# Optimization experiments

Hardware: AMD Instinct MI355X
Metric: run time of the kernel (lower is better)

The kernel has to match this reference:

```python
import jax, jax.numpy as jnp
import numpy as np

H = W = 128
C = 256
NC = 15
BASE_SIZE = 8.0
SCALE = 4.0
RING = np.array([0, 1, 2, 5, 8, 7, 6, 3])  # clockwise ring of 3x3 kernel (row-major idx)
BIAS_CLS = float(-np.log((1.0 - 0.01) / 0.01))  # bias_init_with_prob(0.01)


def conv(x, w, b, pad):
    y = jax.lax.conv_general_dilated(x, w, (1, 1), [(pad, pad), (pad, pad)],
                                     dimension_numbers=('NCHW', 'OIHW', 'NCHW'))
    return y + b[None, :, None, None]


def conv_relu(x, w, b):
    return jax.nn.relu(conv(x, w, b, 1))


def gen_grid_anchors(h, w, stride):
    # AnchorGeneratorRotated: base anchor centered at 0.5*(base_size-1), shifted by stride grid
    ctr = 0.5 * (BASE_SIZE - 1.0)
    gx = jnp.arange(w, dtype=jnp.float32) * stride
    gy = jnp.arange(h, dtype=jnp.float32) * stride
    yy, xx = jnp.meshgrid(gy, gx, indexing='ij')  # row-major (y outer, x inner)
    size = BASE_SIZE * SCALE
    return jnp.stack([xx + ctr, yy + ctr,
                      jnp.full_like(xx, size), jnp.full_like(xx, size),
                      jnp.zeros_like(xx)], axis=-1).reshape(-1, 5)


def norm_angle(a):
    PI = np.pi
    return ((a + PI / 4.0) % PI) - PI / 4.0  # into [-pi/4, 3pi/4)


def rboxes_decode(anchors, deltas, wh_ratio_clip=1e-6):
    # anchors [HW,5], deltas [N,HW,5] -> [N,HW,5]
    max_ratio = float(np.abs(np.log(wh_ratio_clip)))
    dx, dy, dw, dh, dt = [deltas[..., i] for i in range(5)]
    dw = jnp.clip(dw, -max_ratio, max_ratio)
    dh = jnp.clip(dh, -max_ratio, max_ratio)
    ax, ay, aw, ah, aa = [anchors[..., i] for i in range(5)]
    cos, sin = jnp.cos(aa), jnp.sin(aa)
    gx = dx * aw * cos - dy * ah * sin + ax
    gy = dx * aw * sin + dy * ah * cos + ay
    gw = aw * jnp.exp(dw)
    gh = ah * jnp.exp(dh)
    ga = norm_angle(aa + dt)
    return jnp.stack([gx, gy, gw, gh, ga], axis=-1)


def bilinear_sample(x, ys, xs):
    # x [N,C,H,W]; ys/xs [N,H,W,K] float pixel coords -> [N,C,H,W,K], zero outside
    N, Cc, h, w = x.shape
    K = ys.shape[-1]
    x0 = jnp.floor(xs)
    y0 = jnp.floor(ys)
    wx1 = xs - x0
    wx0 = 1.0 - wx1
    wy1 = ys - y0
    wy0 = 1.0 - wy1
    xf = x.reshape(N, Cc, h * w)

    def gather(yi, wy, xi, wxx):
        valid = (yi >= 0) & (yi < h) & (xi >= 0) & (xi < w)
        yc = jnp.clip(yi, 0, h - 1).astype(jnp.int32)
        xc = jnp.clip(xi, 0, w - 1).astype(jnp.int32)
        idx = (yc * w + xc).reshape(N, -1)  # [N,H*W*K]
        v = jax.vmap(lambda xi_, ii_: jnp.take(xi_, ii_, axis=1))(xf, idx)
        v = v.reshape(N, Cc, h, w, K)
        wgt = jnp.where(valid, wy * wxx, 0.0)[:, None]  # [N,1,H,W,K]
        return v * wgt

    out = gather(y0, wy0, x0, wx0)
    out = out + gather(y0, wy0, x0 + 1.0, wx1)
    out = out + gather(y0 + 1.0, wy1, x0, wx0)
    out = out + gather(y0 + 1.0, wy1, x0 + 1.0, wx1)
    return out


def align_conv(x, refine_anchor, stride, w, b):
    # deformable 3x3 conv; sampling grid from refined rotated anchors
    N, Cc, h, ww = x.shape
    k = 3
    idx = jnp.arange(-1, 2, dtype=x.dtype)
    yy, xx = jnp.meshgrid(idx, idx, indexing='ij')
    xx = xx.reshape(-1)
    yy = yy.reshape(-1)  # [9] kernel offsets, row-major matching OIHW flatten
    axc, ayc, aw, ah, aa = [refine_anchor[..., i] for i in range(5)]
    s = jnp.asarray(stride, x.dtype)
    axc, ayc, aw, ah = axc / s, ayc / s, aw / s, ah / s
    cos, sin = jnp.cos(aa), jnp.sin(aa)
    dx = (aw / k)[..., None] * xx  # [N,h,w,9]
    dy = (ah / k)[..., None] * yy
    xs = cos[..., None] * dx - sin[..., None] * dy + axc[..., None]
    ys = sin[..., None] * dx + cos[..., None] * dy + ayc[..., None]
    sampled = bilinear_sample(x, ys, xs)  # [N,C,h,w,9]
    out = jnp.einsum('nchwk,ock->nohw', sampled, w.reshape(w.shape[0], Cc, 9))
    return jax.nn.relu(out + b[None, :, None, None])


def or_conv(x, w, b):
    # ORConv2d(256->32, arf_config=(1,8)): 8 spatially-rotated copies of each 3x3 filter
    o, ci = w.shape[0], w.shape[1]
    wf = w.reshape(o, ci, 9)
    rotated = []
    for r in range(8):
        src = np.arange(9)
        for j in range(8):
            src[RING[j]] = RING[(j - r) % 8]  # rotate ring by r*45deg, center fixed
        rotated.append(wf[..., src])
    wr = jnp.stack(rotated, axis=1).reshape(o * 8, ci, 3, 3)  # channel = o*8 + r
    br = jnp.repeat(b, 8)
    return conv(x, wr, br, 1)


def setup_inputs() -> dict:
    key = jax.random.key(0)
    ks = iter(jax.random.split(key, 32))
    d = {}
    d['feats'] = jax.random.normal(next(ks), (1, C, H, W), dtype=jnp.float32)
    def wlike(shape):
        return 0.01 * jax.random.normal(next(ks), shape, dtype=jnp.float32)
    d['fam_reg_w0'] = wlike((C, C, 3, 3)); d['fam_reg_b0'] = jnp.zeros((C,), jnp.float32)
    d['fam_reg_w1'] = wlike((C, C, 3, 3)); d['fam_reg_b1'] = jnp.zeros((C,), jnp.float32)
    d['fam_reg_hw'] = wlike((5, C, 1, 1)); d['fam_reg_hb'] = jnp.zeros((5,), jnp.float32)
    d['fam_cls_w0'] = wlike((C, C, 3, 3)); d['fam_cls_b0'] = jnp.zeros((C,), jnp.float32)
    d['fam_cls_w1'] = wlike((C, C, 3, 3)); d['fam_cls_b1'] = jnp.zeros((C,), jnp.float32)
    d['fam_cls_hw'] = wlike((NC, C, 1, 1)); d['fam_cls_hb'] = jnp.full((NC,), BIAS_CLS, jnp.float32)
    d['align_w'] = wlike((C, C, 3, 3)); d['align_b'] = jnp.zeros((C,), jnp.float32)
    d['or_w'] = wlike((C // 8, C, 3, 3)); d['or_b'] = jnp.zeros((C // 8,), jnp.float32)
    d['odm_reg_w0'] = wlike((C, C, 3, 3)); d['odm_reg_b0'] = jnp.zeros((C,), jnp.float32)
    d['odm_reg_w1'] = wlike((C, C, 3, 3)); d['odm_reg_b1'] = jnp.zeros((C,), jnp.float32)
    d['odm_reg_hw'] = wlike((5, C, 3, 3)); d['odm_reg_hb'] = jnp.zeros((5,), jnp.float32)
    d['odm_cls_w0'] = wlike((C, C // 8, 3, 3)); d['odm_cls_b0'] = jnp.zeros((C,), jnp.float32)
    d['odm_cls_w1'] = wlike((C, C, 3, 3)); d['odm_cls_b1'] = jnp.zeros((C,), jnp.float32)
    d['odm_cls_hw'] = wlike((NC, C, 3, 3)); d['odm_cls_hb'] = jnp.full((NC,), BIAS_CLS, jnp.float32)
    d['stride'] = 8
    return d


def reference(feats, fam_reg_w0, fam_reg_b0, fam_reg_w1, fam_reg_b1, fam_reg_hw, fam_reg_hb,
              fam_cls_w0, fam_cls_b0, fam_cls_w1, fam_cls_b1, fam_cls_hw, fam_cls_hb,
              align_w, align_b, or_w, or_b,
              odm_reg_w0, odm_reg_b0, odm_reg_w1, odm_reg_b1, odm_reg_hw, odm_reg_hb,
              odm_cls_w0, odm_cls_b0, odm_cls_w1, odm_cls_b1, odm_cls_hw, odm_cls_hb,
              stride):
    x = feats
    t = conv_relu(conv_relu(x, fam_reg_w0, fam_reg_b0), fam_reg_w1, fam_reg_b1)
    fam_bbox_pred = conv(t, fam_reg_hw, fam_reg_hb, 0)  # [N,5,h,w]
    t = conv_relu(conv_relu(x, fam_cls_w0, fam_cls_b0), fam_cls_w1, fam_cls_b1)
    fam_cls_pred = conv(t, fam_cls_hw, fam_cls_hb, 0)   # [N,NC,h,w]
    N, _, h, w = fam_bbox_pred.shape
    anchors = gen_grid_anchors(h, w, stride)  # [h*w,5]
    deltas = jax.lax.stop_gradient(fam_bbox_pred).transpose(0, 2, 3, 1).reshape(N, -1, 5)
    refine_anchor = rboxes_decode(anchors, deltas).reshape(N, h, w, 5)
    al = align_conv(x, refine_anchor, stride, align_w, align_b)  # [N,256,h,w]
    orf = or_conv(al, or_w, or_b)                                # [N,256,h,w]
    pooled = orf.reshape(N, -1, 8, h, w).max(axis=2)             # rotation-invariant pooling -> [N,32,h,w]
    t = conv_relu(conv_relu(pooled, odm_cls_w0, odm_cls_b0), odm_cls_w1, odm_cls_b1)
    odm_cls_pred = conv(t, odm_cls_hw, odm_cls_hb, 1)
    t = conv_relu(conv_relu(orf, odm_reg_w0, odm_reg_b0), odm_reg_w1, odm_reg_b1)
    odm_bbox_pred = conv(t, odm_reg_hw, odm_reg_hb, 1)
    return (fam_cls_pred, fam_bbox_pred, odm_cls_pred, odm_bbox_pred, anchors, refine_anchor)
```

## Files before the change

### kernel.cpp

```cpp
#include <hip/hip_runtime.h>
#include <hip/hip_bf16.h>
#include <hip/hip_fp16.h>

#define HW 128
#define NPX 16384
#define CC 256

typedef short  bf16x8  __attribute__((ext_vector_type(8)));
typedef short  short4v __attribute__((ext_vector_type(4)));
typedef float  f32x4   __attribute__((ext_vector_type(4)));
typedef unsigned int u32x4 __attribute__((ext_vector_type(4)));

static __device__ __forceinline__ short f2bs(float v) {
    union { float f; unsigned u; } x; x.f = v;
    unsigned r = x.u + 0x7FFFu + ((x.u >> 16) & 1u);
    return (short)(r >> 16);
}
static __device__ __forceinline__ float bs2f(short s) {
    union { unsigned u; float f; } x; x.u = ((unsigned)(unsigned short)s) << 16;
    return x.f;
}

static __device__ __forceinline__ int bx_swz() {
    return ((blockIdx.x & 7) << 5) | (blockIdx.x >> 3);
}

struct F8 { unsigned char b; };
__device__ __forceinline__ unsigned char enc8(float v) {
    unsigned short u = __half_as_ushort(__float2half(v));
    unsigned short s = u & 0x8000, mag = u & 0x7FFF;
    mag = (unsigned short)(mag + 0x0080);
    return (unsigned char)((unsigned short)(s | mag) >> 8);
}
__device__ __forceinline__ float dec8(F8 v) {
    return __half2float(__ushort_as_half((unsigned short)(v.b) << 8));
}
__device__ __forceinline__ float ldg_(const float* p) { return *p; }
__device__ __forceinline__ float ldg_(const F8* p)    { return dec8(*p); }

__constant__ int c_ROT9[8][9] = {
    {0,1,2,3,4,5,6,7,8},
    {3,0,1,6,4,2,7,8,5},
    {6,3,0,7,4,1,8,5,2},
    {7,6,3,8,4,0,5,2,1},
    {8,7,6,5,4,3,2,1,0},
    {5,8,7,2,4,6,1,0,3},
    {2,5,8,1,4,7,0,3,6},
    {1,2,5,0,4,8,3,6,7},
};

__device__ __forceinline__ void v9_decode_px(
    const float* bbox, int px, float s,
    float& gx, float& gy, float& gw, float& gh, float& ga)
{
    int y = px >> 7, x = px & 127;
    float ax = x * s + 3.5f, ay = y * s + 3.5f;
    float dx = bbox[0 * NPX + px];
    float dy = bbox[1 * NPX + px];
    float dw = bbox[2 * NPX + px];
    float dh = bbox[3 * NPX + px];
    float dt = bbox[4 * NPX + px];
    const float maxr = 13.815510558f;
    dw = fminf(fmaxf(dw, -maxr), maxr);
    dh = fminf(fmaxf(dh, -maxr), maxr);
    gx = dx * 32.f + ax;
    gy = dy * 32.f + ay;
    gw = 32.f * expf(dw);
    gh = 32.f * expf(dh);
    const float PI = 3.14159265358979323846f;
    float m = fmodf(dt + PI * 0.25f, PI);
    if (m < 0.f) m += PI;
    ga = m - PI * 0.25f;
}


__global__ __launch_bounds__(256) void v10_transpose(
    const float* __restrict__ f, short* __restrict__ xt)
{
    __shared__ float tile[32][33];
    int px0 = blockIdx.x * 32, ci0 = blockIdx.y * 32;
    int tx = threadIdx.x & 31, ty = threadIdx.x >> 5;
#pragma unroll
    for (int i = 0; i < 4; ++i) {
        int ci = ty + i * 8;
        tile[ci][tx] = f[(size_t)(ci0 + ci) * NPX + px0 + tx];
    }
    __syncthreads();
#pragma unroll
    for (int i = 0; i < 4; ++i) {
        int pxr = ty + i * 8;
        xt[(size_t)(px0 + pxr) * 256 + ci0 + tx] = f2bs(tile[tx][pxr]);
    }
}
// ... 126 lines not shown
#pragma unroll
        for (int i = 0; i < 4; ++i)
            if (lofs[i] >= 0) *(bf16x8*)(&S[lofs[i]]) = st[i];
    }
    bf16x8 a[9][OCG];
#pragma unroll
    for (int t = (ONLY1 ? 4 : 0); t < (ONLY1 ? 5 : 9); ++t)
#pragma unroll
        for (int g = 0; g < OCG; ++g)
            a[t][g] = *(const bf16x8*)(wb +
                ((size_t)(t * OCP + ocw + g * 16 + l15) * CIN + quad * 8));
    __syncthreads();

    const int NST = CIN / 32;
    int cur = 0;
    for (int s = 0; s < NST; ++s) {
        const int cib = s * 32;

        bf16x8 st[4];
        if (s + 1 < NST) {
#pragma unroll
            for (int i = 0; i < 4; ++i) {
                st[i] = zf;
                if (gofs[i] >= 0)
                    st[i] = *(const bf16x8*)(xin + gofs[i] + cib + 32);
            }
        }

#pragma unroll
        for (int t = (ONLY1 ? 4 : 0); t < (ONLY1 ? 5 : 9); ++t) {
            const int r = t / 3, dxk = t % 3 - 1;
#pragma unroll
            for (int p = 0; p < 4; ++p) {
                int c = 1 + p * 16 + l15 + dxk;
                bf16x8 b = *(const bf16x8*)(&S[cur * 7920 + (r * 66 + c) * 40 + quad * 8]);
#pragma unroll
                for (int g = 0; g < OCG; ++g)
                    acc[p][g] = __builtin_amdgcn_mfma_f32_16x16x32_bf16(a[t][g], b, acc[p][g], 0, 0, 0);
            }
            if (s + 1 < NST) {
#pragma unroll
                for (int g = 0; g < OCG; ++g)
                    a[t][g] = *(const bf16x8*)(wb +
                        ((size_t)(t * OCP + ocw + g * 16 + l15) * CIN + cib + 32 + quad * 8));
            }
        }

        if (s + 1 < NST) {
#pragma unroll
            for (int i = 0; i < 4; ++i)
                if (lofs[i] >= 0) *(bf16x8*)(&S[(cur ^ 1) * 7920 + lofs[i]]) = st[i];
        }
        __syncthreads();
        cur ^= 1;
    }

#pragma unroll
    for (int p = 0; p < 4; ++p) {
        const int px = y * HW + xh + p * 16 + l15;
#pragma unroll
        for (int g = 0; g < OCG; ++g) {
            const int ocq = ocw + g * 16 + quad * 4;
            if (HEAD) {
                float* o = (float*)outv;
#pragma unroll
                for (int r = 0; r < 4; ++r)
                    if (ocq + r < CoutAct)
                        o[(size_t)(ocq + r) * NPX + px] = acc[p][g][r] + bb[ocq + r];
            } else {
                short4v s4;
#pragma unroll
                for (int r = 0; r < 4; ++r) {
                    float v = acc[p][g][r] + bb[ocq + r];
                    if (RELU) v = fmaxf(v, 0.f);
                    s4[r] = f2bs(v);
                }
                *(short4v*)((short*)outv + (size_t)px * 256 + ocq) = s4;
            }
        }
    }
}

template <int RELU, int CIN>
__device__ __forceinline__ void conv_body4(
    short* S,
    const short* __restrict__ xin, const short* __restrict__ wb,
    const float* __restrict__ bb, short* __restrict__ outb, int bx)
{
    const int y    = bx >> 1;
    const int xh   = (bx & 1) * 64;
    const int tid  = threadIdx.x;
    const int wv   = tid >> 6;
    const int lane = tid & 63;
    const int quad = lane >> 4;
    const int l15  = lane & 15;
    const int ocw  = wv * 64;

    int gofs[4], lofs[4];
#pragma unroll
    for (int i = 0; i < 4; ++i) {
        int e = tid + i * 256;
        gofs[i] = -1; lofs[i] = -1;
        if (e < 792) {
            int pos = e >> 2, part = e & 3;
            int r = pos / 66, c = pos - r * 66;
            int yy = y - 1 + r, xx = xh - 1 + c;
            lofs[i] = (r * 66 + c) * 40 + part * 8;
            if (yy >= 0 && yy < HW && xx >= 0 && xx < HW)
                gofs[i] = (yy * HW + xx) * CIN + part * 8;
        }
    }
    const bf16x8 zf = (bf16x8){0, 0, 0, 0, 0, 0, 0, 0};

    f32x4 acc[4][4];
#pragma unroll
    for (int p = 0; p < 4; ++p)
#pragma unroll
        for (int g = 0; g < 4; ++g) acc[p][g] = (f32x4){0.f, 0.f, 0.f, 0.f};

    {
        bf16x8 st[4];
#pragma unroll
        for (int i = 0; i < 4; ++i) {
            st[i] = zf;
            if (gofs[i] >= 0) st[i] = *(const bf16x8*)(xin + gofs[i]);
        }
#pragma unroll
        for (int i = 0; i < 4; ++i)
            if (lofs[i] >= 0) *(bf16x8*)(&S[lofs[i]]) = st[i];
    }
    bf16x8 aC[4], aN[4];
#pragma unroll
    for (int g = 0; g < 4; ++g)
        aC[g] = *(const bf16x8*)(wb +
            ((size_t)(ocw + g * 16 + l15) * CIN + quad * 8));
#pragma unroll
    for (int g = 0; g < 4; ++g) aN[g] = aC[g];
    __syncthreads();

    const int NST = CIN / 32;
    int cur = 0;
    for (int s = 0; s < NST; ++s) {
        const int cib = s * 32;

        bf16x8 st[4];
        if (s + 1 < NST) {
#pragma unroll
            for (int i = 0; i < 4; ++i) {
                st[i] = zf;
                if (gofs[i] >= 0)
                    st[i] = *(const bf16x8*)(xin + gofs[i] + cib + 32);
            }
        }

#pragma unroll
        for (int t = 0; t < 9; ++t) {
            const int nt   = (t == 8) ? 0 : t + 1;
            const int ncib = (t == 8) ? cib + 32 : cib;
            if (!(s == NST - 1 && t == 8)) {
#pragma unroll
                for (int g = 0; g < 4; ++g)
                    aN[g] = *(const bf16x8*)(wb +
                        ((size_t)(nt * 256 + ocw + g * 16 + l15) * CIN + ncib + quad * 8));
            }
            const int r = t / 3, dxk = t % 3 - 1;
#pragma unroll
            for (int p = 0; p < 4; ++p) {
                int c = 1 + p * 16 + l15 + dxk;
                bf16x8 b = *(const bf16x8*)(&S[cur * 7920 + (r * 66 + c) * 40 + quad * 8]);
#pragma unroll
                for (int g = 0; g < 4; ++g)
                    acc[p][g] = __builtin_amdgcn_mfma_f32_16x16x32_bf16(aC[g], b, acc[p][g], 0, 0, 0);
            }
#pragma unroll
            for (int g = 0; g < 4; ++g) aC[g] = aN[g];
        }

        if (s + 1 < NST) {
#pragma unroll
            for (int i = 0; i < 4; ++i)
                if (lofs[i] >= 0) *(bf16x8*)(&S[(cur ^ 1) * 7920 + lofs[i]]) = st[i];
        }
        __syncthreads();
        cur ^= 1;
    }

#pragma unroll
    for (int p = 0; p < 4; ++p) {
        const int px = y * HW + xh + p * 16 + l15;
#pragma unroll
        for (int g = 0; g < 4; ++g) {
            const int ocq = ocw + g * 16 + quad * 4;
            short4v s4;
#pragma unroll
            for (int r = 0; r < 4; ++r) {
                float v = acc[p][g][r] + bb[ocq + r];
                if (RELU) v = fmaxf(v, 0.f);
                s4[r] = f2bs(v);
            }
            *(short4v*)(outb + (size_t)px * 256 + ocq) = s4;
        }
    }
}

template <int RELU, int HEAD, int ONLY1, int CIN, int OCG>
__global__ __launch_bounds__(256) void v13_conv(
    const short* __restrict__ xin, const short* __restrict__ wb,
    const float* __restrict__ bb, void* __restrict__ outv,
    int CoutAct, int OCP)
{
    __shared__ short S[2 * 7920];
    conv_body<RELU, HEAD, ONLY1, CIN, OCG>(S, xin, wb, bb, outv,
                                           CoutAct, OCP, bx_swz(), blockIdx.y);
}

template <int RELU, int HEAD, int ONLY1, int CIN0, int CIN1, int OCG, int NY, int OCP>
__global__ __launch_bounds__(256) void v13_pair(
    const short* __restrict__ in0, const short* __restrict__ in1,
    const short* __restrict__ wb0, const short* __restrict__ wb1,
    const float* __restrict__ bb0, const float* __restrict__ bb1,
    void* __restrict__ out0, void* __restrict__ out1,
    int cout0, int cout1)
{
    __shared__ short S[2 * 7920];
    const int ybr = blockIdx.y;
    if (ybr < NY)
        conv_body<RELU, HEAD, ONLY1, CIN0, OCG>(S, in0, wb0, bb0, out0,
                                                cout0, OCP, bx_swz(), ybr);
    else
        conv_body<RELU, HEAD, ONLY1, CIN1, OCG>(S, in1, wb1, bb1, out1,
                                                cout1, OCP, bx_swz(), ybr - NY);
}

template <int RELU, int CIN>
__global__ __launch_bounds__(256) __attribute__((amdgpu_waves_per_eu(2, 2)))
void v14_conv(
    const short* __restrict__ xin, const short* __restrict__ wb,
    const float* __restrict__ bb, short* __restrict__ outb)
{
    __shared__ short S[2 * 7920];
    conv_body4<RELU, CIN>(S, xin, wb, bb, outb, bx_swz());
}

template <int RELU, int CIN0, int CIN1>
__global__ __launch_bounds__(256) __attribute__((amdgpu_waves_per_eu(2, 2)))
void v14_pair(
    const short* __restrict__ in0, const short* __restrict__ in1,
    const short* __restrict__ wb0, const short* __restrict__ wb1,
    const float* __restrict__ bb0, const float* __restrict__ bb1,
    short* __restrict__ out0, short* __restrict__ out1)
{
    __shared__ short S[2 * 7920];
    if (blockIdx.y == 0)
        conv_body4<RELU, CIN0>(S, in0, wb0, bb0, out0, bx_swz());
    else
        conv_body4<RELU, CIN1>(S, in1, wb1, bb1, out1, bx_swz());
}

__global__ __launch_bounds__(256) void v13_align(
    const short* __restrict__ xt, const float* __restrict__ bbox,
    const short* __restrict__ wb, const float* __restrict__ bb,
    const int* __restrict__ stride_p, short* __restrict__ outa)
{
    const int bx   = bx_swz();
    const int y    = bx >> 1;
    const int xh   = (bx & 1) * 64;
    const int ocb  = blockIdx.y * 128;
    const int tid  = threadIdx.x;
    const int wv   = tid >> 6, lane = tid & 63, quad = lane >> 4, l15 = lane & 15;
    const int ocw  = ocb + wv * 32;

    __shared__ int   s_idx[4][576];
    __shared__ float s_wgt[4][576];
    __shared__ short S[2][64 * 40];

    const float s = (float)(*stride_p);
    for (int e = tid; e < 576; e += 256) {
        int t = e >> 6, xi = e & 63;
        int px = y * HW + xh + xi;
        float gx, gy, gw, gh, ga;
        v9_decode_px(bbox, px, s, gx, gy, gw, gh, ga);
        float axc = gx / s, ayc = gy / s;
        float aw3 = gw / (3.f * s), ah3 = gh / (3.f * s);
        float cs = cosf(ga), sn = sinf(ga);
        float kx = (float)(t % 3 - 1), ky = (float)(t / 3 - 1);
        float ddx = aw3 * kx, ddy = ah3 * ky;
        float xf = cs * ddx - sn * ddy + axc;
        float yf = sn * ddx + cs * ddy + ayc;
        float fx = floorf(xf), fy = floorf(yf);
        int ix = (int)fx, iy = (int)fy;
        float wx1 = xf - fx, wx0 = 1.f - wx1;
        float wy1 = yf - fy, wy0 = 1.f - wy1;
        bool x0v = (ix >= 0) && (ix < HW), x1v = (ix + 1 >= 0) && (ix + 1 < HW);
        bool y0v = (iy >= 0) && (iy < HW), y1v = (iy + 1 >= 0) && (iy + 1 < HW);
        int x0c = min(max(ix, 0), HW - 1), x1c = min(max(ix + 1, 0), HW - 1);
        int y0c = min(max(iy, 0), HW - 1), y1c = min(max(iy + 1, 0), HW - 1);
        s_idx[0][e] = y0c * HW + x0c;
        s_idx[1][e] = y0c * HW + x1c;
        s_idx[2][e] = y1c * HW + x0c;
        s_idx[3][e] = y1c * HW + x1c;
        s_wgt[0][e] = (y0v && x0v) ? wy0 * wx0 : 0.f;
        s_wgt[1][e] = (y0v && x1v) ? wy0 * wx1 : 0.f;
        s_wgt[2][e] = (y1v && x0v) ? wy1 * wx0 : 0.f;
        s_wgt[3][e] = (y1v && x1v) ? wy1 * wx1 : 0.f;
    }

    f32x4 acc[4][2];
#pragma unroll
    for (int p = 0; p < 4; ++p) { acc[p][0] = (f32x4){0,0,0,0}; acc[p][1] = (f32x4){0,0,0,0}; }

    const int spx = tid >> 2;
    const int sq  = tid & 3;
    const int sw  = spx * 40 + sq * 8;
    const bf16x8 zf = (bf16x8){0, 0, 0, 0, 0, 0, 0, 0};

    __syncthreads();

    bf16x8 aC0, aC1;
    bf16x8 gN0, gN1, gN2, gN3;
    float  wN0, wN1, wN2, wN3;
    {
        int e = spx;
        int i0 = s_idx[0][e], i1 = s_idx[1][e], i2 = s_idx[2][e], i3 = s_idx[3][e];
        float w0 = s_wgt[0][e], w1 = s_wgt[1][e], w2 = s_wgt[2][e], w3 = s_wgt[3][e];
        const short* base = xt + sq * 8;
        bf16x8 g0 = *(const bf16x8*)(base + (size_t)i0 * 256);
        bf16x8 g1 = *(const bf16x8*)(base + (size_t)i1 * 256);
        bf16x8 g2 = *(const bf16x8*)(base + (size_t)i2 * 256);
        bf16x8 g3 = *(const bf16x8*)(base + (size_t)i3 * 256);
        float v[8];
#pragma unroll
        for (int i = 0; i < 8; ++i)
            v[i] = w0 * bs2f(g0[i]) + w1 * bs2f(g1[i]) + w2 * bs2f(g2[i]) + w3 * bs2f(g3[i]);
        u32x4 r;
#pragma unroll
        for (int i = 0; i < 4; ++i)
            asm("v_cvt_pk_bf16_f32 %0, %1, %2" : "=v"(r[i]) : "v"(v[2 * i]), "v"(v[2 * i + 1]));
        *(u32x4*)(&S[0][sw]) = r;
    }
// ... 286 lines not shown
            bool xv1 = (ix + 1 >= 0) && (ix + 1 < HW);
            bool yv0 = (iy >= 0) && (iy < HW);
            bool yv1 = (iy + 1 >= 0) && (iy + 1 < HW);
            if (yv0 && xv0) v += ip[iy * HW + ix] * wy0 * wx0;
            if (yv0 && xv1) v += ip[iy * HW + ix + 1] * wy0 * wx1;
            if (yv1 && xv0) v += ip[(iy + 1) * HW + ix] * wy1 * wx0;
            if (yv1 && xv1) v += ip[(iy + 1) * HW + ix + 1] * wy1 * wx1;
            smp[t >> 7][t & 127] = v;
        }
        __syncthreads();

        float wv[4][9];
#pragma unroll
        for (int i = 0; i < 4; ++i) {
            const float* wp = w + ((size_t)(oc0 + i) * CC + ci) * 9;
#pragma unroll
            for (int k = 0; k < 9; ++k) wv[i][k] = wp[k];
        }
#pragma unroll
        for (int k = 0; k < 9; ++k) {
            float iv[8];
#pragma unroll
            for (int j = 0; j < 8; ++j) iv[j] = smp[k][x0 + j];
#pragma unroll
            for (int i = 0; i < 4; ++i)
#pragma unroll
                for (int j = 0; j < 8; ++j)
                    acc[i][j] += iv[j] * wv[i][k];
        }
    }
#pragma unroll
    for (int i = 0; i < 4; ++i) {
        float b = bias[oc0 + i];
#pragma unroll
        for (int j = 0; j < 8; ++j)
            out[(size_t)(oc0 + i) * NPX + y * HW + x0 + j].b =
                enc8(fmaxf(acc[i][j] + b, 0.f));
    }
}

__global__ __launch_bounds__(256) void v9_pool(
    const F8* __restrict__ orf, F8* __restrict__ pooled)
{
    int g = blockIdx.x * 256 + threadIdx.x;
    if (g >= 32 * NPX) return;
    int px = g & (NPX - 1);
    int c  = g >> 14;
    float m = -3.4e38f;
#pragma unroll
    for (int r = 0; r < 8; ++r)
        m = fmaxf(m, dec8(orf[(size_t)(c * 8 + r) * NPX + px]));
    pooled[g].b = enc8(m);
}

extern "C" void kernel_launch(void* const* d_in, const int* in_sizes, int n_in,
                              void* d_out, int out_size, void* d_ws, size_t ws_size,
                              hipStream_t stream)
{
    const float* feats = (const float*)d_in[0];
    const float* frw0 = (const float*)d_in[1];  const float* frb0 = (const float*)d_in[2];
    const float* frw1 = (const float*)d_in[3];  const float* frb1 = (const float*)d_in[4];
    const float* frhw = (const float*)d_in[5];  const float* frhb = (const float*)d_in[6];
    const float* fcw0 = (const float*)d_in[7];  const float* fcb0 = (const float*)d_in[8];
    const float* fcw1 = (const float*)d_in[9];  const float* fcb1 = (const float*)d_in[10];
    const float* fchw = (const float*)d_in[11]; const float* fchb = (const float*)d_in[12];
    const float* alw  = (const float*)d_in[13]; const float* alb  = (const float*)d_in[14];
    const float* orw  = (const float*)d_in[15]; const float* orb  = (const float*)d_in[16];
    const float* drw0 = (const float*)d_in[17]; const float* drb0 = (const float*)d_in[18];
    const float* drw1 = (const float*)d_in[19]; const float* drb1 = (const float*)d_in[20];
    const float* drhw = (const float*)d_in[21]; const float* drhb = (const float*)d_in[22];
    const float* dcw0 = (const float*)d_in[23]; const float* dcb0 = (const float*)d_in[24];
    const float* dcw1 = (const float*)d_in[25]; const float* dcb1 = (const float*)d_in[26];
    const float* dchw = (const float*)d_in[27]; const float* dchb = (const float*)d_in[28];
    const int*  stride_p = (const int*)d_in[29];

    float* out = (float*)d_out;
    float* o_fam_cls  = out;
    float* o_fam_bbox = out + 245760;
    float* o_odm_cls  = out + 327680;
    float* o_odm_bbox = out + 573440;
    float* o_anchors  = out + 655360;
    float* o_refine   = out + 737280;

    dim3 blk(256);

    const size_t NEED3     = 55097344;
    const size_t NEED2     = 38172672;
    const size_t NEED_FAST = 27395072;
    const size_t NEED_V9   = 8912896;

    if (ws_size >= NEED3) {
        char* ws = (char*)d_ws;
        short* xt = (short*)(ws + 0);
        short* T0 = (short*)(ws + 8388608);
        short* T1 = (short*)(ws + 16777216);
        short* T2 = (short*)(ws + 25165824);
        short* T3 = (short*)(ws + 33554432);
        short* P  = (short*)(ws + 41943040);
        short* WA = (short*)(ws + 42991616);
        float* BA = (float*)(ws + 55083008);

        v12_prepall<<<dim3(2304, 14), blk, 0, stream>>>(
            frw0, frw1, fcw0, fcw1, alw, orw, drw0, drw1, dcw1,
            frhw, fchw, drhw, dchw, dcw0,
            frb0, frb1, fcb0, fcb1, alb, orb, drb0, drb1, dcb1,
            frhb, fchb, drhb, dchb, dcb0,
            WA, BA);
        v10_transpose<<<dim3(512, 8), blk, 0, stream>>>(feats, xt);

        v14_pair<1, 256, 256><<<dim3(256, 2), blk, 0, stream>>>(
            xt, xt, WA + 0, WA + 1179648, BA + 0 * 256, BA + 2 * 256, T0, T2);
        v14_pair<1, 256, 256><<<dim3(256, 2), blk, 0, stream>>>(
            T0, T2, WA + 589824, WA + 1769472, BA + 1 * 256, BA + 3 * 256, T1, T3);
        v13_pair<0, 1, 1, 256, 256, 1, 1, 64><<<dim3(256, 2), blk, 0, stream>>>(
            T1, T3, WA + 5308416, WA + 5455872, BA + 9 * 256, BA + 10 * 256,
            o_fam_bbox, o_fam_cls, 5, 15);
        v9_decode<<<dim3(64), blk, 0, stream>>>(o_fam_bbox, o_anchors, o_refine, stride_p);
        v13_align<<<dim3(256, 2), blk, 0, stream>>>(xt, o_fam_bbox, WA + 2359296, BA + 4 * 256, stride_p, T0);
        v14_conv<0, 256><<<dim3(256, 1), blk, 0, stream>>>(T0, WA + 2949120, BA + 5 * 256, T1);
        v10_pool<<<dim3(2048), blk, 0, stream>>>(T1, P);
        v14_pair<1, 256, 32><<<dim3(256, 2), blk, 0, stream>>>(
            T1, P, WA + 3538944, WA + 5898240, BA + 6 * 256, BA + 13 * 256, T0, T2);
        v14_pair<1, 256, 256><<<dim3(256, 2), blk, 0, stream>>>(
            T0, T2, WA + 4128768, WA + 4718592, BA + 7 * 256, BA + 8 * 256, T1, T3);
        v13_pair<0, 1, 0, 256, 256, 1, 1, 64><<<dim3(256, 2), blk, 0, stream>>>(
            T1, T3, WA + 5603328, WA + 5750784, BA + 11 * 256, BA + 12 * 256,
            o_odm_bbox, o_odm_cls, 5, 15);
    } else if (ws_size >= NEED2) {
        char* ws = (char*)d_ws;
        short* xt = (short*)(ws + 0);
        short* T0 = (short*)(ws + 8388608);
        short* T1 = (short*)(ws + 16777216);
        short* P  = (short*)(ws + 25165824);
        short* WA = (short*)(ws + 26214400);
        float* BA = (float*)(ws + 38158336);

        dim3 gc(256, 2), gh(256, 1);

        v12_prepall<<<dim3(2304, 14), blk, 0, stream>>>(
            frw0, frw1, fcw0, fcw1, alw, orw, drw0, drw1, dcw1,
            frhw, fchw, drhw, dchw, dcw0,
            frb0, frb1, fcb0, fcb1, alb, orb, drb0, drb1, dcb1,
            frhb, fchb, drhb, dchb, dcb0,
            WA, BA);
        v10_transpose<<<dim3(512, 8), blk, 0, stream>>>(feats, xt);

        v13_conv<1, 0, 0, 256, 2><<<gc, blk, 0, stream>>>(xt, WA + 0,       BA + 0 * 256, T0, 256, 256);
        v13_conv<1, 0, 0, 256, 2><<<gc, blk, 0, stream>>>(T0, WA + 589824,  BA + 1 * 256, T1, 256, 256);
        v13_conv<0, 1, 1, 256, 1><<<gh, blk, 0, stream>>>(T1, WA + 5308416, BA + 9 * 256, o_fam_bbox, 5, 64);
        v13_conv<1, 0, 0, 256, 2><<<gc, blk, 0, stream>>>(xt, WA + 1179648, BA + 2 * 256, T0, 256, 256);
        v13_conv<1, 0, 0, 256, 2><<<gc, blk, 0, stream>>>(T0, WA + 1769472, BA + 3 * 256, T1, 256, 256);
        v13_conv<0, 1, 1, 256, 1><<<gh, blk, 0, stream>>>(T1, WA + 5455872, BA + 10 * 256, o_fam_cls, 15, 64);
        v9_decode<<<dim3(64), blk, 0, stream>>>(o_fam_bbox, o_anchors, o_refine, stride_p);
        v13_align<<<dim3(256, 2), blk, 0, stream>>>(xt, o_fam_bbox, WA + 2359296, BA + 4 * 256, stride_p, T0);
        v13_conv<0, 0, 0, 256, 2><<<gc, blk, 0, stream>>>(T0, WA + 2949120, BA + 5 * 256, T1, 256, 256);
        v10_pool<<<dim3(2048), blk, 0, stream>>>(T1, P);
        v13_conv<1, 0, 0, 256, 2><<<gc, blk, 0, stream>>>(T1, WA + 3538944, BA + 6 * 256, T0, 256, 256);
        v13_conv<1, 0, 0, 256, 2><<<gc, blk, 0, stream>>>(T0, WA + 4128768, BA + 7 * 256, T1, 256, 256);
        v13_conv<0, 1, 0, 256, 1><<<gh, blk, 0, stream>>>(T1, WA + 5603328, BA + 11 * 256, o_odm_bbox, 5, 64);
        v13_conv<1, 0, 0, 32, 2><<<gc, blk, 0, stream>>>(P, WA + 5898240, BA + 13 * 256, T0, 256, 256);
        v13_conv<1, 0, 0, 256, 2><<<gc, blk, 0, stream>>>(T0, WA + 4718592, BA + 8 * 256, T1, 256, 256);
        v13_conv<0, 1, 0, 256, 1><<<gh, blk, 0, stream>>>(T1, WA + 5750784, BA + 12 * 256, o_odm_cls, 15, 64);
    } else if (ws_size >= NEED_FAST) {
        char* ws = (char*)d_ws;
        short* xt = (short*)(ws + 0);
        short* T0 = (short*)(ws + 8388608);
        short* T1 = (short*)(ws + 16777216);
        short* P  = (short*)(ws + 25165824);
        short* WB = (short*)(ws + 26214400);
        float* BB = (float*)(ws + 27394048);

        dim3 gc(256, 2), gh(256, 1);

        v10_transpose<<<dim3(512, 8), blk, 0, stream>>>(feats, xt);

#define PREP(W, B, COUT, CIN, OCP, MODE) \
        v10_prep<<<dim3((9 * (OCP) * (CIN) + 255) / 256), blk, 0, stream>>>( \
            W, B, WB, BB, COUT, CIN, OCP, MODE)

        PREP(frw0, frb0, 256, 256, 256, 0);
        v13_conv<1, 0, 0, 256, 2><<<gc, blk, 0, stream>>>(xt, WB, BB, T0, 256, 256);
        PREP(frw1, frb1, 256, 256, 256, 0);
        v13_conv<1, 0, 0, 256, 2><<<gc, blk, 0, stream>>>(T0, WB, BB, T1, 256, 256);
        PREP(frhw, frhb, 5, 256, 64, 2);
        v13_conv<0, 1, 1, 256, 1><<<gh, blk, 0, stream>>>(T1, WB, BB, o_fam_bbox, 5, 64);
        PREP(fcw0, fcb0, 256, 256, 256, 0);
        v13_conv<1, 0, 0, 256, 2><<<gc, blk, 0, stream>>>(xt, WB, BB, T0, 256, 256);
        PREP(fcw1, fcb1, 256, 256, 256, 0);
        v13_conv<1, 0, 0, 256, 2><<<gc, blk, 0, stream>>>(T0, WB, BB, T1, 256, 256);
        PREP(fchw, fchb, 15, 256, 64, 2);
        v13_conv<0, 1, 1, 256, 1><<<gh, blk, 0, stream>>>(T1, WB, BB, o_fam_cls, 15, 64);
        v9_decode<<<dim3(64), blk, 0, stream>>>(o_fam_bbox, o_anchors, o_refine, stride_p);
        PREP(alw, alb, 256, 256, 256, 0);
        v13_align<<<dim3(256, 2), blk, 0, stream>>>(xt, o_fam_bbox, WB, BB, stride_p, T0);
        PREP(orw, orb, 256, 256, 256, 1);
        v13_conv<0, 0, 0, 256, 2><<<gc, blk, 0, stream>>>(T0, WB, BB, T1, 256, 256);
        v10_pool<<<dim3(2048), blk, 0, stream>>>(T1, P);
        PREP(drw0, drb0, 256, 256, 256, 0);
        v13_conv<1, 0, 0, 256, 2><<<gc, blk, 0, stream>>>(T1, WB, BB, T0, 256, 256);
        PREP(drw1, drb1, 256, 256, 256, 0);
        v13_conv<1, 0, 0, 256, 2><<<gc, blk, 0, stream>>>(T0, WB, BB, T1, 256, 256);
        PREP(drhw, drhb, 5, 256, 64, 0);
        v13_conv<0, 1, 0, 256, 1><<<gh, blk, 0, stream>>>(T1, WB, BB, o_odm_bbox, 5, 64);
        PREP(dcw0, dcb0, 256, 32, 256, 0);
        v13_conv<1, 0, 0, 32, 2><<<gc, blk, 0, stream>>>(P, WB, BB, T0, 256, 256);
        PREP(dcw1, dcb1, 256, 256, 256, 0);
// ... 29 lines not shown
```

Before: 550.3 us.

## Split 3x3 conv tile across eight waves with 32 output channels each

The 3x3 conv body moves from 4 waves of 64 output channels each to 8 waves (512 threads) of 32 channels each. Each wave now keeps half the accumulators and weight registers, and the launch bounds and waves-per-EU hints are raised to allow more resident waves. Each pixel fragment read from LDS now feeds only two MFMAs instead of four, so LDS traffic per FLOP doubles, and weight loads per block are spread over more waves. The goal is better latency hiding through higher occupancy, at the cost of less register-level reuse.

```diff
diff --git a/kernel.cpp b/kernel.cpp
--- a/kernel.cpp
+++ b/kernel.cpp
@@ -301,7 +301,7 @@
 }
 
 template <int RELU, int CIN>
-__device__ __forceinline__ void conv_body4(
+__device__ __forceinline__ void conv_body8(
     short* S,
     const short* __restrict__ xin, const short* __restrict__ wb,
     const float* __restrict__ bb, short* __restrict__ outb, int bx)
@@ -313,12 +313,12 @@
     const int lane = tid & 63;
     const int quad = lane >> 4;
     const int l15  = lane & 15;
-    const int ocw  = wv * 64;
-
-    int gofs[4], lofs[4];
-#pragma unroll
-    for (int i = 0; i < 4; ++i) {
-        int e = tid + i * 256;
+    const int ocw  = wv * 32;
+
+    int gofs[2], lofs[2];
+#pragma unroll
+    for (int i = 0; i < 2; ++i) {
+        int e = tid + i * 512;
         gofs[i] = -1; lofs[i] = -1;
         if (e < 792) {
             int pos = e >> 2, part = e & 3;
@@ -331,30 +331,30 @@
     }
     const bf16x8 zf = (bf16x8){0, 0, 0, 0, 0, 0, 0, 0};
 
-    f32x4 acc[4][4];
-#pragma unroll
-    for (int p = 0; p < 4; ++p)
-#pragma unroll
-        for (int g = 0; g < 4; ++g) acc[p][g] = (f32x4){0.f, 0.f, 0.f, 0.f};
+    f32x4 acc[4][2];
+#pragma unroll
+    for (int p = 0; p < 4; ++p) {
+        acc[p][0] = (f32x4){0.f, 0.f, 0.f, 0.f};
+        acc[p][1] = (f32x4){0.f, 0.f, 0.f, 0.f};
+    }
 
     {
-        bf16x8 st[4];
-#pragma unroll
-        for (int i = 0; i < 4; ++i) {
+        bf16x8 st[2];
+#pragma unroll
+        for (int i = 0; i < 2; ++i) {
             st[i] = zf;
             if (gofs[i] >= 0) st[i] = *(const bf16x8*)(xin + gofs[i]);
         }
 #pragma unroll
-        for (int i = 0; i < 4; ++i)
+        for (int i = 0; i < 2; ++i)
             if (lofs[i] >= 0) *(bf16x8*)(&S[lofs[i]]) = st[i];
     }
-    bf16x8 aC[4], aN[4];
-#pragma unroll
-    for (int g = 0; g < 4; ++g)
+    bf16x8 aC[2], aN[2];
+#pragma unroll
+    for (int g = 0; g < 2; ++g)
         aC[g] = *(const bf16x8*)(wb +
             ((size_t)(ocw + g * 16 + l15) * CIN + quad * 8));
-#pragma unroll
-    for (int g = 0; g < 4; ++g) aN[g] = aC[g];
+    aN[0] = aC[0]; aN[1] = aC[1];
     __syncthreads();
 
     const int NST = CIN / 32;
@@ -362,10 +362,10 @@
     for (int s = 0; s < NST; ++s) {
         const int cib = s * 32;
 
-        bf16x8 st[4];
+        bf16x8 st[2];
         if (s + 1 < NST) {
 #pragma unroll
-            for (int i = 0; i < 4; ++i) {
+            for (int i = 0; i < 2; ++i) {
                 st[i] = zf;
                 if (gofs[i] >= 0)
                     st[i] = *(const bf16x8*)(xin + gofs[i] + cib + 32);
@@ -378,7 +378,7 @@
             const int ncib = (t == 8) ? cib + 32 : cib;
             if (!(s == NST - 1 && t == 8)) {
 #pragma unroll
-                for (int g = 0; g < 4; ++g)
+                for (int g = 0; g < 2; ++g)
                     aN[g] = *(const bf16x8*)(wb +
                         ((size_t)(nt * 256 + ocw + g * 16 + l15) * CIN + ncib + quad * 8));
             }
@@ -387,17 +387,15 @@
             for (int p = 0; p < 4; ++p) {
                 int c = 1 + p * 16 + l15 + dxk;
                 bf16x8 b = *(const bf16x8*)(&S[cur * 7920 + (r * 66 + c) * 40 + quad * 8]);
-#pragma unroll
-                for (int g = 0; g < 4; ++g)
-                    acc[p][g] = __builtin_amdgcn_mfma_f32_16x16x32_bf16(aC[g], b, acc[p][g], 0, 0, 0);
-            }
-#pragma unroll
-            for (int g = 0; g < 4; ++g) aC[g] = aN[g];
+                acc[p][0] = __builtin_amdgcn_mfma_f32_16x16x32_bf16(aC[0], b, acc[p][0], 0, 0, 0);
+                acc[p][1] = __builtin_amdgcn_mfma_f32_16x16x32_bf16(aC[1], b, acc[p][1], 0, 0, 0);
+            }
+            aC[0] = aN[0]; aC[1] = aN[1];
         }
 
         if (s + 1 < NST) {
 #pragma unroll
-            for (int i = 0; i < 4; ++i)
+            for (int i = 0; i < 2; ++i)
                 if (lofs[i] >= 0) *(bf16x8*)(&S[(cur ^ 1) * 7920 + lofs[i]]) = st[i];
         }
         __syncthreads();
@@ -408,7 +406,7 @@
     for (int p = 0; p < 4; ++p) {
         const int px = y * HW + xh + p * 16 + l15;
 #pragma unroll
-        for (int g = 0; g < 4; ++g) {
+        for (int g = 0; g < 2; ++g) {
             const int ocq = ocw + g * 16 + quad * 4;
             short4v s4;
 #pragma unroll
@@ -452,18 +450,18 @@
 }
 
 template <int RELU, int CIN>
-__global__ __launch_bounds__(256) __attribute__((amdgpu_waves_per_eu(2, 2)))
-void v14_conv(
+__global__ __launch_bounds__(512) __attribute__((amdgpu_waves_per_eu(4)))
+void v15_conv(
     const short* __restrict__ xin, const short* __restrict__ wb,
     const float* __restrict__ bb, short* __restrict__ outb)
 {
     __shared__ short S[2 * 7920];
-    conv_body4<RELU, CIN>(S, xin, wb, bb, outb, bx_swz());
+    conv_body8<RELU, CIN>(S, xin, wb, bb, outb, bx_swz());
 }
 
 template <int RELU, int CIN0, int CIN1>
-__global__ __launch_bounds__(256) __attribute__((amdgpu_waves_per_eu(2, 2)))
-void v14_pair(
+__global__ __launch_bounds__(512) __attribute__((amdgpu_waves_per_eu(4)))
+void v15_pair(
     const short* __restrict__ in0, const short* __restrict__ in1,
     const short* __restrict__ wb0, const short* __restrict__ wb1,
     const float* __restrict__ bb0, const float* __restrict__ bb1,
@@ -471,9 +469,9 @@
 {
     __shared__ short S[2 * 7920];
     if (blockIdx.y == 0)
-        conv_body4<RELU, CIN0>(S, in0, wb0, bb0, out0, bx_swz());
+        conv_body8<RELU, CIN0>(S, in0, wb0, bb0, out0, bx_swz());
     else
-        conv_body4<RELU, CIN1>(S, in1, wb1, bb1, out1, bx_swz());
+        conv_body8<RELU, CIN1>(S, in1, wb1, bb1, out1, bx_swz());
 }
 
 __global__ __launch_bounds__(256) void v13_align(
@@ -926,7 +924,7 @@
     float* o_anchors  = out + 655360;
     float* o_refine   = out + 737280;
 
-    dim3 blk(256);
+    dim3 blk(256), blk8(512);
 
     const size_t NEED3     = 55097344;
     const size_t NEED2     = 38172672;
@@ -952,20 +950,20 @@
             WA, BA);
         v10_transpose<<<dim3(512, 8), blk, 0, stream>>>(feats, xt);
 
-        v14_pair<1, 256, 256><<<dim3(256, 2), blk, 0, stream>>>(
+        v15_pair<1, 256, 256><<<dim3(256, 2), blk8, 0, stream>>>(
             xt, xt, WA + 0, WA + 1179648, BA + 0 * 256, BA + 2 * 256, T0, T2);
-        v14_pair<1, 256, 256><<<dim3(256, 2), blk, 0, stream>>>(
+        v15_pair<1, 256, 256><<<dim3(256, 2), blk8, 0, stream>>>(
             T0, T2, WA + 589824, WA + 1769472, BA + 1 * 256, BA + 3 * 256, T1, T3);
         v13_pair<0, 1, 1, 256, 256, 1, 1, 64><<<dim3(256, 2), blk, 0, stream>>>(
             T1, T3, WA + 5308416, WA + 5455872, BA + 9 * 256, BA + 10 * 256,
             o_fam_bbox, o_fam_cls, 5, 15);
         v9_decode<<<dim3(64), blk, 0, stream>>>(o_fam_bbox, o_anchors, o_refine, stride_p);
         v13_align<<<dim3(256, 2), blk, 0, stream>>>(xt, o_fam_bbox, WA + 2359296, BA + 4 * 256, stride_p, T0);
-        v14_conv<0, 256><<<dim3(256, 1), blk, 0, stream>>>(T0, WA + 2949120, BA + 5 * 256, T1);
+        v15_conv<0, 256><<<dim3(256, 1), blk8, 0, stream>>>(T0, WA + 2949120, BA + 5 * 256, T1);
         v10_pool<<<dim3(2048), blk, 0, stream>>>(T1, P);
-        v14_pair<1, 256, 32><<<dim3(256, 2), blk, 0, stream>>>(
+        v15_pair<1, 256, 32><<<dim3(256, 2), blk8, 0, stream>>>(
             T1, P, WA + 3538944, WA + 5898240, BA + 6 * 256, BA + 13 * 256, T0, T2);
-        v14_pair<1, 256, 256><<<dim3(256, 2), blk, 0, stream>>>(
+        v15_pair<1, 256, 256><<<dim3(256, 2), blk8, 0, stream>>>(
             T0, T2, WA + 4128768, WA + 4718592, BA + 7 * 256, BA + 8 * 256, T1, T3);
         v13_pair<0, 1, 0, 256, 256, 1, 1, 64><<<dim3(256, 2), blk, 0, stream>>>(
             T1, T3, WA + 5603328, WA + 5750784, BA + 11 * 256, BA + 12 * 256,
```

New measurement: 541.9 us (median of 6 runs). Within noise of the previous version (-1.5%).

## Switch 3x3 conv body to 32x32x16 MFMA and split output channels across blocks

Applied to the files above, without the earlier changes.

The main 256-channel 3x3 conv body moves from 16x16x32 bf16 MFMA tiles (4 pixel groups x 4 channel groups per wave) to 32x32x16 MFMA tiles. Each wave now covers 32 pixels x 64 output channels, and the grid's y dimension doubles so each block handles 128 output channels instead of 256. This cuts accumulator registers per wave and drops the waves_per_eu(2,2) attribute, aiming for higher occupancy and fewer LDS reads per MFMA. The cost is twice as many blocks, each reloading the same input halo tile into LDS, which doubles input traffic.

```diff
diff --git a/kernel.cpp b/kernel.cpp
--- a/kernel.cpp
+++ b/kernel.cpp
@@ -9,6 +9,7 @@
 typedef short  bf16x8  __attribute__((ext_vector_type(8)));
 typedef short  short4v __attribute__((ext_vector_type(4)));
 typedef float  f32x4   __attribute__((ext_vector_type(4)));
+typedef float  f32x16  __attribute__((ext_vector_type(16)));
 typedef unsigned int u32x4 __attribute__((ext_vector_type(4)));
 
 static __device__ __forceinline__ short f2bs(float v) {
@@ -301,19 +302,21 @@
 }
 
 template <int RELU, int CIN>
-__device__ __forceinline__ void conv_body4(
+__device__ __forceinline__ void conv_body16(
     short* S,
     const short* __restrict__ xin, const short* __restrict__ wb,
-    const float* __restrict__ bb, short* __restrict__ outb, int bx)
+    const float* __restrict__ bb, short* __restrict__ outb, int bx, int oy)
 {
     const int y    = bx >> 1;
     const int xh   = (bx & 1) * 64;
     const int tid  = threadIdx.x;
     const int wv   = tid >> 6;
+    const int pg   = wv & 1;
+    const int og   = wv >> 1;
     const int lane = tid & 63;
-    const int quad = lane >> 4;
-    const int l15  = lane & 15;
-    const int ocw  = wv * 64;
+    const int l31  = lane & 31;
+    const int hi   = lane >> 5;
+    const int ocw  = oy * 128 + og * 64;
 
     int gofs[4], lofs[4];
 #pragma unroll
@@ -330,12 +333,8 @@
         }
     }
     const bf16x8 zf = (bf16x8){0, 0, 0, 0, 0, 0, 0, 0};
-
-    f32x4 acc[4][4];
-#pragma unroll
-    for (int p = 0; p < 4; ++p)
-#pragma unroll
-        for (int g = 0; g < 4; ++g) acc[p][g] = (f32x4){0.f, 0.f, 0.f, 0.f};
+    const f32x16 z16 = {0,0,0,0, 0,0,0,0, 0,0,0,0, 0,0,0,0};
+    f32x16 acc0 = z16, acc1 = z16;
 
     {
         bf16x8 st[4];
@@ -350,11 +349,12 @@
     }
     bf16x8 aC[4], aN[4];
 #pragma unroll
-    for (int g = 0; g < 4; ++g)
-        aC[g] = *(const bf16x8*)(wb +
-            ((size_t)(ocw + g * 16 + l15) * CIN + quad * 8));
-#pragma unroll
-    for (int g = 0; g < 4; ++g) aN[g] = aC[g];
+    for (int k = 0; k < 2; ++k)
+#pragma unroll
+        for (int j = 0; j < 2; ++j)
+            aC[k * 2 + j] = *(const bf16x8*)(wb +
+                ((size_t)(ocw + j * 32 + l31) * CIN + k * 16 + hi * 8));
+    aN[0] = aC[0]; aN[1] = aC[1]; aN[2] = aC[2]; aN[3] = aC[3];
     __syncthreads();
 
     const int NST = CIN / 32;
@@ -378,21 +378,21 @@
             const int ncib = (t == 8) ? cib + 32 : cib;
             if (!(s == NST - 1 && t == 8)) {
 #pragma unroll
-                for (int g = 0; g < 4; ++g)
-                    aN[g] = *(const bf16x8*)(wb +
-                        ((size_t)(nt * 256 + ocw + g * 16 + l15) * CIN + ncib + quad * 8));
+                for (int k = 0; k < 2; ++k)
+#pragma unroll
+                    for (int j = 0; j < 2; ++j)
+                        aN[k * 2 + j] = *(const bf16x8*)(wb +
+                            ((size_t)(nt * 256 + ocw + j * 32 + l31) * CIN + ncib + k * 16 + hi * 8));
             }
             const int r = t / 3, dxk = t % 3 - 1;
-#pragma unroll
-            for (int p = 0; p < 4; ++p) {
-                int c = 1 + p * 16 + l15 + dxk;
-                bf16x8 b = *(const bf16x8*)(&S[cur * 7920 + (r * 66 + c) * 40 + quad * 8]);
-#pragma unroll
-                for (int g = 0; g < 4; ++g)
-                    acc[p][g] = __builtin_amdgcn_mfma_f32_16x16x32_bf16(aC[g], b, acc[p][g], 0, 0, 0);
-            }
-#pragma unroll
-            for (int g = 0; g < 4; ++g) aC[g] = aN[g];
+            const int posb = (r * 66 + 1 + pg * 32 + l31 + dxk) * 40 + hi * 8;
+#pragma unroll
+            for (int k = 0; k < 2; ++k) {
+                bf16x8 b = *(const bf16x8*)(&S[cur * 7920 + posb + k * 16]);
+                acc0 = __builtin_amdgcn_mfma_f32_32x32x16_bf16(aC[k * 2 + 0], b, acc0, 0, 0, 0);
+                acc1 = __builtin_amdgcn_mfma_f32_32x32x16_bf16(aC[k * 2 + 1], b, acc1, 0, 0, 0);
+            }
+            aC[0] = aN[0]; aC[1] = aN[1]; aC[2] = aN[2]; aC[3] = aN[3];
         }
 
         if (s + 1 < NST) {
@@ -404,18 +404,19 @@
         cur ^= 1;
     }
 
-#pragma unroll
-    for (int p = 0; p < 4; ++p) {
-        const int px = y * HW + xh + p * 16 + l15;
-#pragma unroll
-        for (int g = 0; g < 4; ++g) {
-            const int ocq = ocw + g * 16 + quad * 4;
+    const int px = y * HW + xh + pg * 32 + l31;
+#pragma unroll
+    for (int j = 0; j < 2; ++j) {
+        const f32x16 a = j ? acc1 : acc0;
+#pragma unroll
+        for (int rg = 0; rg < 4; ++rg) {
+            const int ocq = ocw + j * 32 + rg * 8 + hi * 4;
             short4v s4;
 #pragma unroll
-            for (int r = 0; r < 4; ++r) {
-                float v = acc[p][g][r] + bb[ocq + r];
+            for (int i = 0; i < 4; ++i) {
+                float v = a[rg * 4 + i] + bb[ocq + i];
                 if (RELU) v = fmaxf(v, 0.f);
-                s4[r] = f2bs(v);
+                s4[i] = f2bs(v);
             }
             *(short4v*)(outb + (size_t)px * 256 + ocq) = s4;
         }
@@ -452,28 +453,27 @@
 }
 
 template <int RELU, int CIN>
-__global__ __launch_bounds__(256) __attribute__((amdgpu_waves_per_eu(2, 2)))
-void v14_conv(
+__global__ __launch_bounds__(256) void v16_conv(
     const short* __restrict__ xin, const short* __restrict__ wb,
     const float* __restrict__ bb, short* __restrict__ outb)
 {
     __shared__ short S[2 * 7920];
-    conv_body4<RELU, CIN>(S, xin, wb, bb, outb, bx_swz());
+    conv_body16<RELU, CIN>(S, xin, wb, bb, outb, bx_swz(), blockIdx.y);
 }
 
 template <int RELU, int CIN0, int CIN1>
-__global__ __launch_bounds__(256) __attribute__((amdgpu_waves_per_eu(2, 2)))
-void v14_pair(
+__global__ __launch_bounds__(256) void v16_pair(
     const short* __restrict__ in0, const short* __restrict__ in1,
     const short* __restrict__ wb0, const short* __restrict__ wb1,
     const float* __restrict__ bb0, const float* __restrict__ bb1,
     short* __restrict__ out0, short* __restrict__ out1)
 {
     __shared__ short S[2 * 7920];
-    if (blockIdx.y == 0)
-        conv_body4<RELU, CIN0>(S, in0, wb0, bb0, out0, bx_swz());
+    const int ybr = blockIdx.y;
+    if (ybr < 2)
+        conv_body16<RELU, CIN0>(S, in0, wb0, bb0, out0, bx_swz(), ybr);
     else
-        conv_body4<RELU, CIN1>(S, in1, wb1, bb1, out1, bx_swz());
+        conv_body16<RELU, CIN1>(S, in1, wb1, bb1, out1, bx_swz(), ybr - 2);
 }
 
 __global__ __launch_bounds__(256) void v13_align(
@@ -952,20 +952,20 @@
             WA, BA);
         v10_transpose<<<dim3(512, 8), blk, 0, stream>>>(feats, xt);
 
-        v14_pair<1, 256, 256><<<dim3(256, 2), blk, 0, stream>>>(
+        v16_pair<1, 256, 256><<<dim3(256, 4), blk, 0, stream>>>(
             xt, xt, WA + 0, WA + 1179648, BA + 0 * 256, BA + 2 * 256, T0, T2);
-        v14_pair<1, 256, 256><<<dim3(256, 2), blk, 0, stream>>>(
+        v16_pair<1, 256, 256><<<dim3(256, 4), blk, 0, stream>>>(
             T0, T2, WA + 589824, WA + 1769472, BA + 1 * 256, BA + 3 * 256, T1, T3);
         v13_pair<0, 1, 1, 256, 256, 1, 1, 64><<<dim3(256, 2), blk, 0, stream>>>(
             T1, T3, WA + 5308416, WA + 5455872, BA + 9 * 256, BA + 10 * 256,
             o_fam_bbox, o_fam_cls, 5, 15);
         v9_decode<<<dim3(64), blk, 0, stream>>>(o_fam_bbox, o_anchors, o_refine, stride_p);
         v13_align<<<dim3(256, 2), blk, 0, stream>>>(xt, o_fam_bbox, WA + 2359296, BA + 4 * 256, stride_p, T0);
-        v14_conv<0, 256><<<dim3(256, 1), blk, 0, stream>>>(T0, WA + 2949120, BA + 5 * 256, T1);
+        v16_conv<0, 256><<<dim3(256, 2), blk, 0, stream>>>(T0, WA + 2949120, BA + 5 * 256, T1);
         v10_pool<<<dim3(2048), blk, 0, stream>>>(T1, P);
-        v14_pair<1, 256, 32><<<dim3(256, 2), blk, 0, stream>>>(
+        v16_pair<1, 256, 32><<<dim3(256, 4), blk, 0, stream>>>(
             T1, P, WA + 3538944, WA + 5898240, BA + 6 * 256, BA + 13 * 256, T0, T2);
-        v14_pair<1, 256, 256><<<dim3(256, 2), blk, 0, stream>>>(
+        v16_pair<1, 256, 256><<<dim3(256, 4), blk, 0, stream>>>(
             T0, T2, WA + 4128768, WA + 4718592, BA + 7 * 256, BA + 8 * 256, T1, T3);
         v13_pair<0, 1, 0, 256, 256, 1, 1, 64><<<dim3(256, 2), blk, 0, stream>>>(
             T1, T3, WA + 5603328, WA + 5750784, BA + 11 * 256, BA + 12 * 256,
```

Result: slower. 798.1 us (+45.0%).
